# Kernel optimization log

Hardware: AMD Instinct MI355X
Metric: run time of the kernel (lower is better)

The kernel has to match this reference:

```python
import jax, jax.numpy as jnp
import numpy as np

B, S, D, H = 2, 2048, 1024, 16
HD = D // H  # head_dim = 64


def setup_inputs() -> dict:
    key = jax.random.key(0)
    ks = jax.random.split(key, 5)
    scale = 1.0 / np.sqrt(D)
    return {
        "x": jax.random.normal(ks[0], (B, S, D), dtype=jnp.float32),
        "attention_mask": jnp.zeros((B, 1, 1, S), dtype=jnp.float32),
        "Wq": jax.random.normal(ks[1], (D, D), dtype=jnp.float32) * scale,
        "Wk": jax.random.normal(ks[2], (D, D), dtype=jnp.float32) * scale,
        "Wv": jax.random.normal(ks[3], (D, D), dtype=jnp.float32) * scale,
        "Wo": jax.random.normal(ks[4], (D, D), dtype=jnp.float32) * scale,
    }


def reference(x, attention_mask, Wq, Wk, Wv, Wo):
    # nn.Linear applies x @ W.T; weights here stored as [out, in]
    q = jnp.einsum("bsd,ed->bse", x, Wq).reshape(B, S, H, HD).transpose(0, 2, 1, 3)
    k = jnp.einsum("bsd,ed->bse", x, Wk).reshape(B, S, H, HD).transpose(0, 2, 1, 3)
    v = jnp.einsum("bsd,ed->bse", x, Wv).reshape(B, S, H, HD).transpose(0, 2, 1, 3)
    scores = jnp.einsum("bhqd,bhkd->bhqk", q, k) / jnp.sqrt(jnp.float32(HD))
    scores = scores + attention_mask  # additive mask, broadcasts [B,1,1,S]
    attn = jax.nn.softmax(scores, axis=-1)  # dropout p=0 (eval) -> identity
    ctx = jnp.einsum("bhqk,bhkd->bhqd", attn, v)
    ctx = ctx.transpose(0, 2, 1, 3).reshape(B, S, D)
    out = jnp.einsum("bsd,ed->bse", ctx, Wo)
    return out
```

## Files before the change

### kernel.cpp

```cpp
#include <hip/hip_runtime.h>
#include <hip/hip_bf16.h>
#include <cstdint>
#include <cstddef>


#define B_  2
#define S_  2048
#define D_  1024
#define H_  16
#define HD_ 64

typedef __bf16 bf16x8 __attribute__((ext_vector_type(8)));
typedef __bf16 bf16x4 __attribute__((ext_vector_type(4)));
typedef float  f32x4  __attribute__((ext_vector_type(4)));

__device__ __forceinline__ void async16(const __bf16* g, const __bf16* l) {
  __builtin_amdgcn_global_load_lds(
      (const __attribute__((address_space(1))) void*)(uintptr_t)g,
      (__attribute__((address_space(3))) void*)(uint32_t)(uintptr_t)l,
      16, 0, 0);
}

__device__ __forceinline__ unsigned cvt_pk_bf16(float lo, float hi) {
  unsigned r;
  asm("v_cvt_pk_bf16_f32 %0, %1, %2" : "=v"(r) : "v"(lo), "v"(hi));
  return r;
}

__global__ __launch_bounds__(256) void cvt_all(const float* __restrict__ x,
    const float* __restrict__ wq, const float* __restrict__ wk,
    const float* __restrict__ wv, const float* __restrict__ wo,
    __bf16* __restrict__ xb, __bf16* __restrict__ wqb, __bf16* __restrict__ wkb,
    __bf16* __restrict__ wvb, __bf16* __restrict__ wob) {
  const int sel = blockIdx.y;
  const float* src; __bf16* dst; int n;
  if      (sel == 0) { src = x;  dst = xb;  n = B_ * S_ * D_; }
  else if (sel == 1) { src = wq; dst = wqb; n = D_ * D_; }
  else if (sel == 2) { src = wk; dst = wkb; n = D_ * D_; }
  else if (sel == 3) { src = wv; dst = wvb; n = D_ * D_; }
  else               { src = wo; dst = wob; n = D_ * D_; }
  for (int i = blockIdx.x * 256 + threadIdx.x; i * 4 < n; i += gridDim.x * 256) {
    const float4 v = *(const float4*)(src + (size_t)i * 4);
    bf16x4 o;
    o[0] = (__bf16)v.x; o[1] = (__bf16)v.y; o[2] = (__bf16)v.z; o[3] = (__bf16)v.w;
    *(bf16x4*)(dst + (size_t)i * 4) = o;
  }
}

__global__ __launch_bounds__(512, 4) void qkv_gemm(const __bf16* __restrict__ xb,
                                                   const __bf16* __restrict__ wqkv,
                                                   __bf16* __restrict__ qkv) {
  __shared__ __align__(16) char smem[32768];
  __bf16* As = (__bf16*)smem;
  __bf16* Bs = (__bf16*)(smem + 16384);
  __bf16* cs = (__bf16*)smem;

  const int lin = blockIdx.y * 24 + blockIdx.x;
  const int xcd = lin & 7, slot = lin >> 3;
  const int mi = xcd >> 2, ni = xcd & 3;
  const int mB = mi * 16 + slot / 6;
  const int nB = ni * 6  + slot % 6;
  const int m0  = mB * 128;
  const int sel = nB >> 3;
  const int n0s = (nB & 7) * 128;
  const int n0w = nB * 128;
  constexpr int K = D_, N = D_;
  constexpr size_t NTE = (size_t)B_ * S_ * D_;

  const int tid  = threadIdx.x, lane = tid & 63, wave = tid >> 6;
  const int l15  = lane & 15,   quad = lane >> 4;
  const int wr   = wave >> 1,   wc   = wave & 1;

  f32x4 acc[2][4] = {};
  for (int k0 = 0; k0 < K; k0 += 64) {
#pragma unroll
    for (int i = 0; i < 2; ++i) {
      const int e = (wave * 2 + i) * 512 + lane * 8;
      const int row = e >> 6, col = e & 63;
      async16(xb   + (size_t)(m0  + row) * K + k0 + col, As + (wave * 2 + i) * 512);
      async16(wqkv + (size_t)(n0w + row) * K + k0 + col, Bs + (wave * 2 + i) * 512);
    }
    __syncthreads();
#pragma unroll
    for (int kk = 0; kk < 2; ++kk) {
      bf16x8 af[2], bfv[4];
#pragma unroll
      for (int rt = 0; rt < 2; ++rt)
        af[rt] = *(const bf16x8*)(As + (wr * 32 + rt * 16 + l15) * 64 + kk * 32 + quad * 8);
#pragma unroll
      for (int ct = 0; ct < 4; ++ct)
        bfv[ct] = *(const bf16x8*)(Bs + (wc * 64 + ct * 16 + l15) * 64 + kk * 32 + quad * 8);
#pragma unroll
      for (int rt = 0; rt < 2; ++rt)
#pragma unroll
        for (int ct = 0; ct < 4; ++ct)
          acc[rt][ct] = __builtin_amdgcn_mfma_f32_16x16x32_bf16(af[rt], bfv[ct], acc[rt][ct], 0, 0, 0);
    }
    __syncthreads();
  }

  const int b  = m0 >> 11;
  const int s0 = m0 & (S_ - 1);
  __bf16* vtb = qkv + 2 * NTE;
#pragma unroll
  for (int pass = 0; pass < 2; ++pass) {
    __syncthreads();
    if ((wave >> 2) == pass) {
#pragma unroll
      for (int rt = 0; rt < 2; ++rt)
#pragma unroll
        for (int ct = 0; ct < 4; ++ct)
#pragma unroll
          for (int r = 0; r < 4; ++r)
            cs[((wr & 1) * 32 + rt * 16 + quad * 4 + r) * 136 + wc * 64 + ct * 16 + l15] =
                (__bf16)acc[rt][ct][r];
    }
    __syncthreads();
    if (sel < 2) {
      __bf16* C = qkv + (size_t)sel * NTE;
      const int rr = tid >> 3, cb = (tid & 7) * 16;
      const bf16x8 v0 = *(const bf16x8*)(cs + rr * 136 + cb);
      const bf16x8 v1 = *(const bf16x8*)(cs + rr * 136 + cb + 8);
      *(bf16x8*)(C + (size_t)(m0 + pass * 64 + rr) * N + n0s + cb)     = v0;
      *(bf16x8*)(C + (size_t)(m0 + pass * 64 + rr) * N + n0s + cb + 8) = v1;
    } else {
      const int e_loc = tid >> 2, sh = (tid & 3) * 16;
      __bf16* dst = vtb + (size_t)(b * 1024 + n0s + e_loc) * S_ + s0 + pass * 64 + sh;
#pragma unroll
      for (int p2 = 0; p2 < 2; ++p2) {
        bf16x8 v;
#pragma unroll
        for (int j = 0; j < 8; ++j)
          v[j] = cs[(sh + p2 * 8 + j) * 136 + e_loc];
        *(bf16x8*)(dst + p2 * 8) = v;
      }
    }
  }
}

__global__ __launch_bounds__(512, 4) void o_gemm(const __bf16* __restrict__ cb,
                                                 const __bf16* __restrict__ wo,
                                                 float* __restrict__ out) {
  __shared__ __align__(16) __bf16 As[64 * 64];
  __shared__ __align__(16) __bf16 Bs[128 * 64];
  const int lin = blockIdx.y * 8 + blockIdx.x;
  const int xcd = lin & 7, slot = lin >> 3;
  const int mi = xcd >> 1, ni = xcd & 1;
  const int mB = mi * 16 + (slot >> 2);
  const int nB = ni * 4  + (slot & 3);
  const int m0 = mB * 64, n0 = nB * 128;
  constexpr int K = D_, N = D_;
  const int tid  = threadIdx.x, lane = tid & 63, wave = tid >> 6;
  const int l15  = lane & 15,   quad = lane >> 4;
  const int wr   = wave >> 2,   wc   = wave & 3;

  f32x4 acc[2][2] = {};
  for (int k0 = 0; k0 < K; k0 += 64) {
    {
      const int e = wave * 512 + lane * 8;
      const int row = e >> 6, col = e & 63;
      async16(cb + (size_t)(m0 + row) * K + k0 + col, As + wave * 512);
    }
#pragma unroll
    for (int i = 0; i < 2; ++i) {
      const int e = (wave * 2 + i) * 512 + lane * 8;
      const int row = e >> 6, col = e & 63;
      async16(wo + (size_t)(n0 + row) * K + k0 + col, Bs + (wave * 2 + i) * 512);
    }
    __syncthreads();
#pragma unroll
    for (int kk = 0; kk < 2; ++kk) {
      bf16x8 af[2], bfv[2];
#pragma unroll
      for (int rt = 0; rt < 2; ++rt)
        af[rt] = *(const bf16x8*)(As + (wr * 32 + rt * 16 + l15) * 64 + kk * 32 + quad * 8);
#pragma unroll
      for (int ct = 0; ct < 2; ++ct)
        bfv[ct] = *(const bf16x8*)(Bs + (wc * 32 + ct * 16 + l15) * 64 + kk * 32 + quad * 8);
#pragma unroll
      for (int rt = 0; rt < 2; ++rt)
#pragma unroll
        for (int ct = 0; ct < 2; ++ct)
          acc[rt][ct] = __builtin_amdgcn_mfma_f32_16x16x32_bf16(af[rt], bfv[ct], acc[rt][ct], 0, 0, 0);
    }
    __syncthreads();
  }
#pragma unroll
  for (int rt = 0; rt < 2; ++rt)
#pragma unroll
    for (int ct = 0; ct < 2; ++ct)
#pragma unroll
      for (int r = 0; r < 4; ++r) {
        const int row = m0 + wr * 32 + rt * 16 + quad * 4 + r;
        const int col = n0 + wc * 32 + ct * 16 + l15;
        out[(size_t)row * N + col] = acc[rt][ct][r];
      }
}

__global__ __launch_bounds__(512, 4) void attn2(const __bf16* __restrict__ Q,
                                                const __bf16* __restrict__ K,
                                                const __bf16* __restrict__ Vt,
                                                const float* __restrict__ mask,
                                                __bf16* __restrict__ O) {
  constexpr int LKT = 72, LVT = 136;
  __shared__ __align__(16) __bf16 kt[2][128 * LKT];
  __shared__ __align__(16) __bf16 vt[2][64 * LVT];
  __shared__ __align__(16) float  mfull[S_];

  const int tid  = threadIdx.x, lane = tid & 63, wave = tid >> 6;
  const int l15  = lane & 15,   quad = lane >> 4;
  const int b = blockIdx.z, h = blockIdx.y, q0 = blockIdx.x * 128;
  const size_t base   = (size_t)b * S_ * D_ + h * HD_;
  const size_t vtbase = (size_t)(b * H_ + h) * HD_ * S_;
  const int qw = q0 + wave * 16;
  constexpr float LOG2E = 1.44269504088896340736f;
  constexpr float SC    = 0.125f * LOG2E;
  constexpr int  NT     = S_ / 128;

  const int idx0 = tid,        kr0 = idx0 >> 3, kc0 = (idx0 & 7) * 8;
  const int idx1 = 512 + tid,  kr1 = idx1 >> 3, kc1 = (idx1 & 7) * 8;
  const int vr0 = idx0 >> 4, vc0 = (idx0 & 15) * 8;
  const int vr1 = idx1 >> 4, vc1 = (idx1 & 15) * 8;

  bf16x8 qf[2];
#pragma unroll
  for (int kb = 0; kb < 2; ++kb)
    qf[kb] = *(const bf16x8*)(Q + base + (size_t)(qw + l15) * D_ + kb * 32 + quad * 8);

  bf16x8 ones;
#pragma unroll
  for (int j = 0; j < 8; ++j) ones[j] = (__bf16)1.0f;

  float m_run = -1e30f;
  f32x4 oacc[4] = {};
  f32x4 lacc   = {};

  bf16x8 rk0, rk1, rv0, rv1;
  rk0 = *(const bf16x8*)(K + base + (size_t)kr0 * D_ + kc0);
  rk1 = *(const bf16x8*)(K + base + (size_t)kr1 * D_ + kc1);
  rv0 = *(const bf16x8*)(Vt + vtbase + (size_t)vr0 * S_ + vc0);
  rv1 = *(const bf16x8*)(Vt + vtbase + (size_t)vr1 * S_ + vc1);
#pragma unroll
  for (int i = 0; i < S_ / 512; ++i)
    mfull[i * 512 + tid] = mask[(size_t)b * S_ + i * 512 + tid] * LOG2E;
  *(bf16x8*)(&kt[0][kr0 * LKT + kc0]) = rk0;
  *(bf16x8*)(&kt[0][kr1 * LKT + kc1]) = rk1;
  *(bf16x8*)(&vt[0][vr0 * LVT + vc0]) = rv0;
  *(bf16x8*)(&vt[0][vr1 * LVT + vc1]) = rv1;
  __syncthreads();

  for (int t = 0; t < NT; ++t) {
    const int cur = t & 1;
    const int t0  = t * 128;
    const __bf16* ktb = &kt[cur][0];
    const __bf16* vtb = &vt[cur][0];

    if (t + 1 < NT) {
      const int tn = t0 + 128;
      rk0 = *(const bf16x8*)(K + base + (size_t)(tn + kr0) * D_ + kc0);
      rk1 = *(const bf16x8*)(K + base + (size_t)(tn + kr1) * D_ + kc1);
      rv0 = *(const bf16x8*)(Vt + vtbase + (size_t)vr0 * S_ + tn + vc0);
      rv1 = *(const bf16x8*)(Vt + vtbase + (size_t)vr1 * S_ + tn + vc1);
    }

    f32x4 sacc[8] = {};
    __builtin_amdgcn_s_setprio(1);
#pragma unroll
    for (int kti = 0; kti < 8; ++kti) {
      const __bf16* kr = ktb + (kti * 16 + l15) * LKT + quad * 8;
      const bf16x8 a0 = *(const bf16x8*)(kr);
      const bf16x8 a1 = *(const bf16x8*)(kr + 32);
      sacc[kti] = __builtin_amdgcn_mfma_f32_16x16x32_bf16(a0, qf[0], sacc[kti], 0, 0, 0);
      sacc[kti] = __builtin_amdgcn_mfma_f32_16x16x32_bf16(a1, qf[1], sacc[kti], 0, 0, 0);
    }
    __builtin_amdgcn_s_setprio(0);

    f32x4 tm4;
#pragma unroll
    for (int r = 0; r < 4; ++r) tm4[r] = -1e30f;
#pragma unroll
    for (int kti = 0; kti < 8; ++kti) {
      const f32x4 mv = *(const f32x4*)(mfull + t0 + kti * 16 + quad * 4);
#pragma unroll
      for (int r = 0; r < 4; ++r) {
        sacc[kti][r] = sacc[kti][r] * SC + mv[r];
        tm4[r] = fmaxf(tm4[r], sacc[kti][r]);
      }
    }
    float tm = fmaxf(fmaxf(tm4[0], tm4[1]), fmaxf(tm4[2], tm4[3]));
    tm = fmaxf(tm, __shfl_xor(tm, 16));
    tm = fmaxf(tm, __shfl_xor(tm, 32));

    if (!__all(tm <= m_run + 8.f)) {
      const float mnew  = fmaxf(m_run, tm);
      const float alpha = __builtin_amdgcn_exp2f(m_run - mnew);
      m_run = mnew;
#pragma unroll
      for (int r = 0; r < 4; ++r) {
        const float aR = __shfl(alpha, quad * 4 + r);
        lacc[r] *= aR;
#pragma unroll
        for (int nt = 0; nt < 4; ++nt) oacc[nt][r] *= aR;
      }
    }

#pragma unroll
    for (int kb = 0; kb < 4; ++kb) {
      unsigned dd[2][2];
#pragma unroll
      for (int kk = 0; kk < 2; ++kk) {
        const int kti = 2 * kb + kk;
        float p[4];
#pragma unroll
        for (int r = 0; r < 4; ++r)
          p[r] = __builtin_amdgcn_exp2f(sacc[kti][r] - m_run);
        dd[kk][0] = cvt_pk_bf16(p[0], p[1]);
        dd[kk][1] = cvt_pk_bf16(p[2], p[3]);
      }
      unsigned a0 = dd[0][0], b0 = dd[1][0], a1 = dd[0][1], b1 = dd[1][1];
      asm("v_permlane32_swap_b32 %0, %1" : "+v"(a0), "+v"(b0));
      asm("v_permlane16_swap_b32 %0, %1" : "+v"(a0), "+v"(b0));
      asm("v_permlane32_swap_b32 %0, %1" : "+v"(a1), "+v"(b1));
      asm("v_permlane16_swap_b32 %0, %1" : "+v"(a1), "+v"(b1));
      union { unsigned u[4]; bf16x8 v; } pw;
      pw.u[0] = a0; pw.u[1] = a1; pw.u[2] = b0; pw.u[3] = b1;
      const bf16x8 pa = pw.v;
      __builtin_amdgcn_s_setprio(1);
      lacc = __builtin_amdgcn_mfma_f32_16x16x32_bf16(pa, ones, lacc, 0, 0, 0);
#pragma unroll
      for (int nt = 0; nt < 4; ++nt) {
        const bf16x8 vf = *(const bf16x8*)(vtb + (nt * 16 + l15) * LVT + kb * 32 + quad * 8);
        oacc[nt] = __builtin_amdgcn_mfma_f32_16x16x32_bf16(pa, vf, oacc[nt], 0, 0, 0);
      }
      __builtin_amdgcn_s_setprio(0);
    }

    __syncthreads();
    if (t + 1 < NT) {
      const int nxt = cur ^ 1;
      *(bf16x8*)(&kt[nxt][kr0 * LKT + kc0]) = rk0;
      *(bf16x8*)(&kt[nxt][kr1 * LKT + kc1]) = rk1;
      *(bf16x8*)(&vt[nxt][vr0 * LVT + vc0]) = rv0;
      *(bf16x8*)(&vt[nxt][vr1 * LVT + vc1]) = rv1;
    }
    __syncthreads();
  }

#pragma unroll
  for (int r = 0; r < 4; ++r) {
    const float inv = 1.0f / lacc[r];
    const int row = qw + quad * 4 + r;
#pragma unroll
    for (int nt = 0; nt < 4; ++nt)
      O[base + (size_t)row * D_ + nt * 16 + l15] = (__bf16)(oacc[nt][r] * inv);
  }
}

extern "C" void kernel_launch(void* const* d_in, const int* in_sizes, int n_in,
                              void* d_out, int out_size, void* d_ws, size_t ws_size,
                              hipStream_t stream) {
  const float* x    = (const float*)d_in[0];
  const float* mask = (const float*)d_in[1];
  const float* Wq   = (const float*)d_in[2];
  const float* Wk   = (const float*)d_in[3];
  const float* Wv   = (const float*)d_in[4];
  const float* Wo   = (const float*)d_in[5];

  char* ws = (char*)d_ws;
  const size_t MB = 1ull << 20;
  const size_t NT = (size_t)B_ * S_ * D_;
  __bf16* xb  = (__bf16*)(ws);
  __bf16* wqb = (__bf16*)(ws + 8 * MB);
  __bf16* wkb = (__bf16*)(ws + 10 * MB);
  __bf16* wvb = (__bf16*)(ws + 12 * MB);
  __bf16* wob = (__bf16*)(ws + 14 * MB);
  __bf16* qkv = (__bf16*)(ws + 16 * MB);
  __bf16* qb  = qkv;
  __bf16* kb  = qkv + NT;
  __bf16* vtb = qkv + 2 * NT;
  __bf16* cb  = xb;

  cvt_all<<<dim3(1024, 5), 256, 0, stream>>>(x, Wq, Wk, Wv, Wo, xb, wqb, wkb, wvb, wob);
  qkv_gemm<<<dim3(24, 32), 512, 0, stream>>>(xb, wqb, qkv);
  attn2<<<dim3(S_ / 128, H_, B_), 512, 0, stream>>>(qb, kb, vtb, mask, cb);
  o_gemm<<<dim3(8, 64), 512, 0, stream>>>(cb, wob, (float*)d_out);
}
```

Baseline: 208.6 us.

## Double-buffer GEMM LDS tiles and deepen K/V prefetch in attention

Both the QKV and output-projection GEMMs now ping-pong between two LDS buffers. The async global-to-LDS loads for the next K tile are issued before the MFMAs on the current tile, which removes one barrier per iteration. The attention kernel keeps K/V tiles two steps ahead in registers and writes the next tile into LDS before computing on the current one, dropping one __syncthreads per tile. The cost is double the LDS footprint: 64KB per block in qkv_gemm, which caps blocks per CU below the launch bound. It also adds register pressure in attention.

Result: faster. 200.1 us (-4.1%).

```diff
diff --git a/kernel.cpp b/kernel.cpp
--- a/kernel.cpp
+++ b/kernel.cpp
@@ -50,9 +50,7 @@
 __global__ __launch_bounds__(512, 4) void qkv_gemm(const __bf16* __restrict__ xb,
                                                    const __bf16* __restrict__ wqkv,
                                                    __bf16* __restrict__ qkv) {
-  __shared__ __align__(16) char smem[32768];
-  __bf16* As = (__bf16*)smem;
-  __bf16* Bs = (__bf16*)(smem + 16384);
+  __shared__ __align__(16) char smem[65536];
   __bf16* cs = (__bf16*)smem;
 
   const int lin = blockIdx.y * 24 + blockIdx.x;
@@ -71,16 +69,35 @@
   const int l15  = lane & 15,   quad = lane >> 4;
   const int wr   = wave >> 1,   wc   = wave & 1;
 
+  const int e0 = (wave * 2 + 0) * 512 + lane * 8;
+  const int e1 = (wave * 2 + 1) * 512 + lane * 8;
+  const int r0 = e0 >> 6, c0 = e0 & 63, r1 = e1 >> 6, c1 = e1 & 63;
+
   f32x4 acc[2][4] = {};
-  for (int k0 = 0; k0 < K; k0 += 64) {
-#pragma unroll
-    for (int i = 0; i < 2; ++i) {
-      const int e = (wave * 2 + i) * 512 + lane * 8;
-      const int row = e >> 6, col = e & 63;
-      async16(xb   + (size_t)(m0  + row) * K + k0 + col, As + (wave * 2 + i) * 512);
-      async16(wqkv + (size_t)(n0w + row) * K + k0 + col, Bs + (wave * 2 + i) * 512);
-    }
-    __syncthreads();
+
+  {
+    __bf16* As = (__bf16*)(smem);
+    __bf16* Bs = (__bf16*)(smem + 16384);
+    async16(xb   + (size_t)(m0  + r0) * K + c0, As + (wave * 2 + 0) * 512);
+    async16(xb   + (size_t)(m0  + r1) * K + c1, As + (wave * 2 + 1) * 512);
+    async16(wqkv + (size_t)(n0w + r0) * K + c0, Bs + (wave * 2 + 0) * 512);
+    async16(wqkv + (size_t)(n0w + r1) * K + c1, Bs + (wave * 2 + 1) * 512);
+  }
+  __syncthreads();
+
+  for (int t = 0; t < K / 64; ++t) {
+    const int cur = t & 1;
+    if (t + 1 < K / 64) {
+      const int k0 = (t + 1) * 64;
+      __bf16* As = (__bf16*)(smem + (cur ^ 1) * 32768);
+      __bf16* Bs = (__bf16*)(smem + (cur ^ 1) * 32768 + 16384);
+      async16(xb   + (size_t)(m0  + r0) * K + k0 + c0, As + (wave * 2 + 0) * 512);
+      async16(xb   + (size_t)(m0  + r1) * K + k0 + c1, As + (wave * 2 + 1) * 512);
+      async16(wqkv + (size_t)(n0w + r0) * K + k0 + c0, Bs + (wave * 2 + 0) * 512);
+      async16(wqkv + (size_t)(n0w + r1) * K + k0 + c1, Bs + (wave * 2 + 1) * 512);
+    }
+    const __bf16* As = (const __bf16*)(smem + cur * 32768);
+    const __bf16* Bs = (const __bf16*)(smem + cur * 32768 + 16384);
 #pragma unroll
     for (int kk = 0; kk < 2; ++kk) {
       bf16x8 af[2], bfv[4];
@@ -141,8 +158,7 @@
 __global__ __launch_bounds__(512, 4) void o_gemm(const __bf16* __restrict__ cb,
                                                  const __bf16* __restrict__ wo,
                                                  float* __restrict__ out) {
-  __shared__ __align__(16) __bf16 As[64 * 64];
-  __shared__ __align__(16) __bf16 Bs[128 * 64];
+  __shared__ __align__(16) char smem[49152];
   const int lin = blockIdx.y * 8 + blockIdx.x;
   const int xcd = lin & 7, slot = lin >> 3;
   const int mi = xcd >> 1, ni = xcd & 1;
@@ -154,20 +170,34 @@
   const int l15  = lane & 15,   quad = lane >> 4;
   const int wr   = wave >> 2,   wc   = wave & 3;
 
+  const int ea  = wave * 512 + lane * 8;
+  const int ra  = ea >> 6, ca = ea & 63;
+  const int eb0 = (wave * 2 + 0) * 512 + lane * 8;
+  const int eb1 = (wave * 2 + 1) * 512 + lane * 8;
+  const int rb0 = eb0 >> 6, cb0 = eb0 & 63, rb1 = eb1 >> 6, cb1 = eb1 & 63;
+
   f32x4 acc[2][2] = {};
-  for (int k0 = 0; k0 < K; k0 += 64) {
-    {
-      const int e = wave * 512 + lane * 8;
-      const int row = e >> 6, col = e & 63;
-      async16(cb + (size_t)(m0 + row) * K + k0 + col, As + wave * 512);
-    }
-#pragma unroll
-    for (int i = 0; i < 2; ++i) {
-      const int e = (wave * 2 + i) * 512 + lane * 8;
-      const int row = e >> 6, col = e & 63;
-      async16(wo + (size_t)(n0 + row) * K + k0 + col, Bs + (wave * 2 + i) * 512);
-    }
-    __syncthreads();
+  {
+    __bf16* As = (__bf16*)(smem);
+    __bf16* Bs = (__bf16*)(smem + 8192);
+    async16(cb + (size_t)(m0 + ra)  * K + ca,  As + wave * 512);
+    async16(wo + (size_t)(n0 + rb0) * K + cb0, Bs + (wave * 2 + 0) * 512);
+    async16(wo + (size_t)(n0 + rb1) * K + cb1, Bs + (wave * 2 + 1) * 512);
+  }
+  __syncthreads();
+
+  for (int t = 0; t < K / 64; ++t) {
+    const int cur = t & 1;
+    if (t + 1 < K / 64) {
+      const int k0 = (t + 1) * 64;
+      __bf16* As = (__bf16*)(smem + (cur ^ 1) * 24576);
+      __bf16* Bs = (__bf16*)(smem + (cur ^ 1) * 24576 + 8192);
+      async16(cb + (size_t)(m0 + ra)  * K + k0 + ca,  As + wave * 512);
+      async16(wo + (size_t)(n0 + rb0) * K + k0 + cb0, Bs + (wave * 2 + 0) * 512);
+      async16(wo + (size_t)(n0 + rb1) * K + k0 + cb1, Bs + (wave * 2 + 1) * 512);
+    }
+    const __bf16* As = (const __bf16*)(smem + cur * 24576);
+    const __bf16* Bs = (const __bf16*)(smem + cur * 24576 + 8192);
 #pragma unroll
     for (int kk = 0; kk < 2; ++kk) {
       bf16x8 af[2], bfv[2];
@@ -247,6 +277,12 @@
   *(bf16x8*)(&kt[0][kr1 * LKT + kc1]) = rk1;
   *(bf16x8*)(&vt[0][vr0 * LVT + vc0]) = rv0;
   *(bf16x8*)(&vt[0][vr1 * LVT + vc1]) = rv1;
+  if (NT > 1) {
+    rk0 = *(const bf16x8*)(K + base + (size_t)(128 + kr0) * D_ + kc0);
+    rk1 = *(const bf16x8*)(K + base + (size_t)(128 + kr1) * D_ + kc1);
+    rv0 = *(const bf16x8*)(Vt + vtbase + (size_t)vr0 * S_ + 128 + vc0);
+    rv1 = *(const bf16x8*)(Vt + vtbase + (size_t)vr1 * S_ + 128 + vc1);
+  }
   __syncthreads();
 
   for (int t = 0; t < NT; ++t) {
@@ -256,7 +292,14 @@
     const __bf16* vtb = &vt[cur][0];
 
     if (t + 1 < NT) {
-      const int tn = t0 + 128;
+      const int nxt = cur ^ 1;
+      *(bf16x8*)(&kt[nxt][kr0 * LKT + kc0]) = rk0;
+      *(bf16x8*)(&kt[nxt][kr1 * LKT + kc1]) = rk1;
+      *(bf16x8*)(&vt[nxt][vr0 * LVT + vc0]) = rv0;
+      *(bf16x8*)(&vt[nxt][vr1 * LVT + vc1]) = rv1;
+    }
+    if (t + 2 < NT) {
+      const int tn = t0 + 256;
       rk0 = *(const bf16x8*)(K + base + (size_t)(tn + kr0) * D_ + kc0);
       rk1 = *(const bf16x8*)(K + base + (size_t)(tn + kr1) * D_ + kc1);
       rv0 = *(const bf16x8*)(Vt + vtbase + (size_t)vr0 * S_ + tn + vc0);
@@ -335,14 +378,6 @@
       __builtin_amdgcn_s_setprio(0);
     }
 
-    __syncthreads();
-    if (t + 1 < NT) {
-      const int nxt = cur ^ 1;
-      *(bf16x8*)(&kt[nxt][kr0 * LKT + kc0]) = rk0;
-      *(bf16x8*)(&kt[nxt][kr1 * LKT + kc1]) = rk1;
-      *(bf16x8*)(&vt[nxt][vr0 * LVT + vc0]) = rv0;
-      *(bf16x8*)(&vt[nxt][vr1 * LVT + vc1]) = rv1;
-    }
     __syncthreads();
   }
 
```
